# Optimization experiments

Measured on AMD Instinct MI355X. Metric: run time of the kernel, lower is better.

## Reference

```python
import jax, jax.numpy as jnp
import numpy as np

WINDOW = 13

def setup_inputs() -> dict:
    key = jax.random.key(0)
    ks = jax.random.split(key, 5)
    B, C, D, H, W = 8, 64, 13, 64, 64
    c8 = C // 8
    x = jax.random.normal(ks[0], (B, C, D, H, W), dtype=jnp.float32)
    wq = jax.random.normal(ks[1], (c8, C), dtype=jnp.float32) * 0.1
    wk = jax.random.normal(ks[2], (c8, C), dtype=jnp.float32) * 0.1
    wv = jax.random.normal(ks[3], (C, C), dtype=jnp.float32) * 0.1
    bq = jnp.zeros((c8,), jnp.float32)
    bk = jnp.zeros((c8,), jnp.float32)
    bv = jnp.zeros((C,), jnp.float32)
    return {"x": x, "wq": wq, "bq": bq, "wk": wk, "bk": bk, "wv": wv, "bv": bv}

def reference(x, wq, bq, wk, bk, wv, bv):
    B, C, D, H, W = x.shape
    N = D * H * W
    nb = N // WINDOW  # N chosen divisible by WINDOW
    xf = x.reshape(B, C, N)
    # 1x1 Conv3d == per-voxel channel matmul
    q = jnp.einsum('oc,bcn->bon', wq, xf) + bq[None, :, None]
    k = jnp.einsum('oc,bcn->bon', wk, xf) + bk[None, :, None]
    v = jnp.einsum('oc,bcn->bon', wv, xf) + bv[None, :, None]
    # split flattened spatial dim into independent windows of size 13
    qb = q.reshape(B, -1, nb, WINDOW)
    kb = k.reshape(B, -1, nb, WINDOW)
    vb = v.reshape(B, C, nb, WINDOW)
    # scores[b,n,i,j] = sum_c q[b,c,n,i] * k[b,c,n,j]  (no scaling, as in source)
    scores = jnp.einsum('bcni,bcnj->bnij', qb, kb)
    att = jax.nn.softmax(scores, axis=-1)
    # out[b,c,n,i] = sum_j v[b,c,n,j] * att[b,n,i,j]  (v @ att^T per window)
    out = jnp.einsum('bcnj,bnij->bcni', vb, att)
    return out.reshape(B, C, D, H, W)
```

## Files before the change

### kernel.cpp

```cpp
#include <hip/hip_runtime.h>

#define WINDOW 13
#define NTOT   53248
#define WPB    8
#define VT     104
#define VS     112
#define WS     72
#define QKS    112
#define VFS    68

typedef float floatx4 __attribute__((ext_vector_type(4)));
typedef short shortx8 __attribute__((ext_vector_type(8)));

__device__ __forceinline__ unsigned short f2bf(float f) {
    union { float f; unsigned int u; } v; v.f = f;
    unsigned int u = v.u;
    unsigned int r = (u + 0x7fffu + ((u >> 16) & 1u)) >> 16;
    return (unsigned short)r;
}

__device__ __forceinline__ unsigned int pk2(float a, float b) {
    return (unsigned int)f2bf(a) | ((unsigned int)f2bf(b) << 16);
}

__global__ __launch_bounds__(512, 4)
void attn_win13_kernel(const float* __restrict__ x,
                       const float* __restrict__ wq, const float* __restrict__ bq,
                       const float* __restrict__ wk, const float* __restrict__ bk,
                       const float* __restrict__ wv, const float* __restrict__ bv,
                       float* __restrict__ out)
{
    __shared__ __align__(16) unsigned short xT[VS * WS];
    __shared__ __align__(16) unsigned short wbf[80 * WS];
    __shared__ float ball[80];
    __shared__ __align__(16) float vf[VS * VFS];
    __shared__ float qk[16 * QKS];
    __shared__ float att[WPB * 169];

    const int tid = threadIdx.x;
    const int b   = blockIdx.y;
    const int v0  = blockIdx.x * VT;
    const size_t total = (size_t)512 * NTOT;

    if (tid < 224) {
        const int vq = tid >> 3, cg8 = tid & 7;
        const int c0 = cg8 * 8, vx = vq * 4;
        float xv[4][8];
#pragma unroll
        for (int i = 0; i < 8; ++i) {
            size_t idx = (size_t)(b * 64 + c0 + i) * NTOT + v0 + vx;
            if (idx > total - 4) idx = total - 4;
            const float4 t = *(const float4*)(x + idx);
            xv[0][i] = t.x; xv[1][i] = t.y; xv[2][i] = t.z; xv[3][i] = t.w;
        }
#pragma unroll
        for (int r = 0; r < 4; ++r) {
            uint4 pk;
            pk.x = pk2(xv[r][0], xv[r][1]);
            pk.y = pk2(xv[r][2], xv[r][3]);
            pk.z = pk2(xv[r][4], xv[r][5]);
            pk.w = pk2(xv[r][6], xv[r][7]);
            *(uint4*)(&xT[(vx + r) * WS + c0]) = pk;
        }
    } else if (tid >= 256) {
        const int wf0 = tid - 256;
#pragma unroll
        for (int it = 0; it < 3; ++it) {
            const int wf = wf0 + (it << 8);
            if (wf < 640) {
                const int r = wf >> 3, cw = (wf & 7) * 8;
                const float* src = (r < 8)  ? (wq + r * 64 + cw)
                                 : (r < 16) ? (wk + (r - 8) * 64 + cw)
                                            : (wv + (r - 16) * 64 + cw);
                const float4 w0 = *(const float4*)src;
                const float4 w1 = *(const float4*)(src + 4);
                uint4 pk;
                pk.x = pk2(w0.x, w0.y); pk.y = pk2(w0.z, w0.w);
                pk.z = pk2(w1.x, w1.y); pk.w = pk2(w1.z, w1.w);
                *(uint4*)(&wbf[r * WS + cw]) = pk;
            }
        }
    }
    if (tid >= 432) {
        const int t2 = tid - 432;
        ball[t2] = (t2 < 8) ? bq[t2] : (t2 < 16) ? bk[t2 - 8] : bv[t2 - 16];
    }
    __syncthreads();

    {
        const int wid  = tid >> 6;
        const int lane = tid & 63;
        const int col  = lane & 15;
        const int g    = lane >> 4;
        for (int t = wid; t < 35; t += 8) {
            const int mt = t / 7, nt = t % 7;
            const shortx8 a0 = *(const shortx8*)(&wbf[(mt * 16 + col) * WS + g * 8]);
            const shortx8 b0 = *(const shortx8*)(&xT [(nt * 16 + col) * WS + g * 8]);
            const shortx8 a1 = *(const shortx8*)(&wbf[(mt * 16 + col) * WS + 32 + g * 8]);
            const shortx8 b1 = *(const shortx8*)(&xT [(nt * 16 + col) * WS + 32 + g * 8]);
            floatx4 acc = {0.f, 0.f, 0.f, 0.f};
            acc = __builtin_amdgcn_mfma_f32_16x16x32_bf16(a0, b0, acc, 0, 0, 0);
            acc = __builtin_amdgcn_mfma_f32_16x16x32_bf16(a1, b1, acc, 0, 0, 0);
            const int row0 = mt * 16 + g * 4;
            const int vox  = nt * 16 + col;
            if (mt == 0) {
                qk[(row0 + 0) * QKS + vox] = acc[0] + ball[row0 + 0];
                qk[(row0 + 1) * QKS + vox] = acc[1] + ball[row0 + 1];
                qk[(row0 + 2) * QKS + vox] = acc[2] + ball[row0 + 2];
                qk[(row0 + 3) * QKS + vox] = acc[3] + ball[row0 + 3];
            } else {
                const int c0 = row0 - 16;
                float4 st = make_float4(acc[0] + ball[row0 + 0], acc[1] + ball[row0 + 1],
                                        acc[2] + ball[row0 + 2], acc[3] + ball[row0 + 3]);
                *(float4*)(&vf[vox * VFS + c0]) = st;
            }
        }
    }
    __syncthreads();

    for (int f = tid; f < WPB * 169; f += 512) {
        const int w = f / 169, rem = f % 169;
        const int i = rem / 13, j = rem % 13;
        const float* qp = &qk[w * 13 + i];
        const float* kp = &qk[w * 13 + j];
        float s = 0.f;
#pragma unroll
        for (int o = 0; o < 8; ++o)
            s += qp[o * QKS] * kp[(8 + o) * QKS];
        att[f] = s;
    }
    __syncthreads();

    if (tid < WPB * WINDOW) {
        float* row = att + tid * 13;
        float m = row[0];
#pragma unroll
        for (int j = 1; j < 13; ++j) m = fmaxf(m, row[j]);
        float s0 = __expf(row[0] - m), s1 = __expf(row[1] - m), s2 = __expf(row[2] - m);
        float s3 = __expf(row[3] - m), s4 = __expf(row[4] - m), s5 = __expf(row[5] - m);
        float s6 = __expf(row[6] - m), s7 = __expf(row[7] - m), s8 = __expf(row[8] - m);
        float s9 = __expf(row[9] - m), sa = __expf(row[10] - m), sb = __expf(row[11] - m);
        float sc = __expf(row[12] - m);
        const float inv = 1.f / (s0+s1+s2+s3+s4+s5+s6+s7+s8+s9+sa+sb+sc);
        row[0]=s0*inv; row[1]=s1*inv; row[2]=s2*inv; row[3]=s3*inv; row[4]=s4*inv;
        row[5]=s5*inv; row[6]=s6*inv; row[7]=s7*inv; row[8]=s8*inv; row[9]=s9*inv;
        row[10]=sa*inv; row[11]=sb*inv; row[12]=sc*inv;
    }
    __syncthreads();

    for (int f = tid; f < 16 * VT; f += 512) {
        const int cg = f / VT, vx = f % VT;
        const int w = vx / 13, i = vx % 13;
        const float* arow  = att + w * 169 + i * 13;
        const float* vbase = &vf[(w * 13) * VFS + cg * 4];
        float4 o4 = make_float4(0.f, 0.f, 0.f, 0.f);
#pragma unroll
        for (int j = 0; j < 13; ++j) {
            const float a = arow[j];
            const float4 vv = *(const float4*)(vbase + j * VFS);
            o4.x += a * vv.x; o4.y += a * vv.y; o4.z += a * vv.z; o4.w += a * vv.w;
        }
        float* op = out + (size_t)(b * 64 + cg * 4) * NTOT + v0 + vx;
        op[0]                 = o4.x;
        op[(size_t)NTOT]      = o4.y;
        op[(size_t)2 * NTOT]  = o4.z;
        op[(size_t)3 * NTOT]  = o4.w;
    }
}

extern "C" void kernel_launch(void* const* d_in, const int* in_sizes, int n_in,
                              void* d_out, int out_size, void* d_ws, size_t ws_size,
                              hipStream_t stream) {
    const float* x  = (const float*)d_in[0];
    const float* wq = (const float*)d_in[1];
    const float* bq = (const float*)d_in[2];
    const float* wk = (const float*)d_in[3];
    const float* bk = (const float*)d_in[4];
    const float* wv = (const float*)d_in[5];
    const float* bv = (const float*)d_in[6];
    float* out = (float*)d_out;

    dim3 grid(NTOT / VT, 8);
    dim3 block(512);
    attn_win13_kernel<<<grid, block, 0, stream>>>(x, wq, bq, wk, bk, wv, bv, out);
}
```

Before: 235.7 us.

## Store V in bf16 LDS and alias attention buffer to cut LDS footprint

The V projection is now packed to bf16 in shared memory instead of fp32, and the attention buffer reuses the weight staging buffer. Together these shrink LDS use so launch bounds can go from 4 to 6 blocks per CU. The output loop now gives each thread 8 channels instead of 4, halving the loop iterations. In exchange, V carries bf16 rounding error, and the kernel now depends on wbf being dead after the projection step.

```diff
diff --git a/kernel.cpp b/kernel.cpp
--- a/kernel.cpp
+++ b/kernel.cpp
@@ -7,7 +7,6 @@
 #define VS     112
 #define WS     72
 #define QKS    112
-#define VFS    68
 
 typedef float floatx4 __attribute__((ext_vector_type(4)));
 typedef short shortx8 __attribute__((ext_vector_type(8)));
@@ -23,7 +22,14 @@
     return (unsigned int)f2bf(a) | ((unsigned int)f2bf(b) << 16);
 }
 
-__global__ __launch_bounds__(512, 4)
+__device__ __forceinline__ float bflo(unsigned int u) {
+    union { unsigned int u; float f; } v; v.u = u << 16; return v.f;
+}
+__device__ __forceinline__ float bfhi(unsigned int u) {
+    union { unsigned int u; float f; } v; v.u = u & 0xffff0000u; return v.f;
+}
+
+__global__ __launch_bounds__(512, 6)
 void attn_win13_kernel(const float* __restrict__ x,
                        const float* __restrict__ wq, const float* __restrict__ bq,
                        const float* __restrict__ wk, const float* __restrict__ bk,
@@ -33,9 +39,9 @@
     __shared__ __align__(16) unsigned short xT[VS * WS];
     __shared__ __align__(16) unsigned short wbf[80 * WS];
     __shared__ float ball[80];
-    __shared__ __align__(16) float vf[VS * VFS];
-    __shared__ float qk[16 * QKS];
-    __shared__ float att[WPB * 169];
+    __shared__ __align__(16) unsigned short vbf[VT * WS];
+    __shared__ __align__(16) float qk[16 * QKS];
+    float* const att = (float*)wbf;
 
     const int tid = threadIdx.x;
     const int b   = blockIdx.y;
@@ -108,11 +114,12 @@
                 qk[(row0 + 1) * QKS + vox] = acc[1] + ball[row0 + 1];
                 qk[(row0 + 2) * QKS + vox] = acc[2] + ball[row0 + 2];
                 qk[(row0 + 3) * QKS + vox] = acc[3] + ball[row0 + 3];
-            } else {
+            } else if (vox < VT) {
                 const int c0 = row0 - 16;
-                float4 st = make_float4(acc[0] + ball[row0 + 0], acc[1] + ball[row0 + 1],
-                                        acc[2] + ball[row0 + 2], acc[3] + ball[row0 + 3]);
-                *(float4*)(&vf[vox * VFS + c0]) = st;
+                uint2 st;
+                st.x = pk2(acc[0] + ball[row0 + 0], acc[1] + ball[row0 + 1]);
+                st.y = pk2(acc[2] + ball[row0 + 2], acc[3] + ball[row0 + 3]);
+                *(uint2*)(&vbf[vox * WS + c0]) = st;
             }
         }
     }
@@ -148,23 +155,30 @@
     }
     __syncthreads();
 
-    for (int f = tid; f < 16 * VT; f += 512) {
+    for (int f = tid; f < 8 * VT; f += 512) {
         const int cg = f / VT, vx = f % VT;
         const int w = vx / 13, i = vx % 13;
-        const float* arow  = att + w * 169 + i * 13;
-        const float* vbase = &vf[(w * 13) * VFS + cg * 4];
-        float4 o4 = make_float4(0.f, 0.f, 0.f, 0.f);
+        const float* arow = att + w * 169 + i * 13;
+        const unsigned short* vbase = &vbf[(w * 13) * WS + cg * 8];
+        float o0=0.f,o1=0.f,o2=0.f,o3=0.f,o4=0.f,o5=0.f,o6=0.f,o7=0.f;
 #pragma unroll
         for (int j = 0; j < 13; ++j) {
             const float a = arow[j];
-            const float4 vv = *(const float4*)(vbase + j * VFS);
-            o4.x += a * vv.x; o4.y += a * vv.y; o4.z += a * vv.z; o4.w += a * vv.w;
-        }
-        float* op = out + (size_t)(b * 64 + cg * 4) * NTOT + v0 + vx;
-        op[0]                 = o4.x;
-        op[(size_t)NTOT]      = o4.y;
-        op[(size_t)2 * NTOT]  = o4.z;
-        op[(size_t)3 * NTOT]  = o4.w;
+            const uint4 vv = *(const uint4*)(vbase + j * WS);
+            o0 += a * bflo(vv.x); o1 += a * bfhi(vv.x);
+            o2 += a * bflo(vv.y); o3 += a * bfhi(vv.y);
+            o4 += a * bflo(vv.z); o5 += a * bfhi(vv.z);
+            o6 += a * bflo(vv.w); o7 += a * bfhi(vv.w);
+        }
+        float* op = out + (size_t)(b * 64 + cg * 8) * NTOT + v0 + vx;
+        op[0]                 = o0;
+        op[(size_t)NTOT]      = o1;
+        op[(size_t)2 * NTOT]  = o2;
+        op[(size_t)3 * NTOT]  = o3;
+        op[(size_t)4 * NTOT]  = o4;
+        op[(size_t)5 * NTOT]  = o5;
+        op[(size_t)6 * NTOT]  = o6;
+        op[(size_t)7 * NTOT]  = o7;
     }
 }
 
```

New measurement: 229.9 us. -2.4%, faster.

## Compute attention-weighted V with bf16 MFMA and shrink shared memory for occupancy

Applied to the files above, without the earlier changes.

Stores V projections as bf16 in a padded per-window layout and writes softmax probabilities as zero-padded bf16 rows. The final out = V·attᵀ product then runs on 16x16x32 MFMA (one wave per window) instead of a scalar FMA loop. It also reuses the weight and qk buffers for the score and probability arrays, which cuts LDS per block and allows launch bounds to be raised to 6 blocks. The trade-off is lower precision for V and the attention weights, plus some redundant padded MFMA work.

```diff
diff --git a/kernel.cpp b/kernel.cpp
--- a/kernel.cpp
+++ b/kernel.cpp
@@ -7,7 +7,7 @@
 #define VS     112
 #define WS     72
 #define QKS    112
-#define VFS    68
+#define VPS    132
 
 typedef float floatx4 __attribute__((ext_vector_type(4)));
 typedef short shortx8 __attribute__((ext_vector_type(8)));
@@ -23,7 +23,7 @@
     return (unsigned int)f2bf(a) | ((unsigned int)f2bf(b) << 16);
 }
 
-__global__ __launch_bounds__(512, 4)
+__global__ __launch_bounds__(512, 6)
 void attn_win13_kernel(const float* __restrict__ x,
                        const float* __restrict__ wq, const float* __restrict__ bq,
                        const float* __restrict__ wk, const float* __restrict__ bk,
@@ -33,9 +33,10 @@
     __shared__ __align__(16) unsigned short xT[VS * WS];
     __shared__ __align__(16) unsigned short wbf[80 * WS];
     __shared__ float ball[80];
-    __shared__ __align__(16) float vf[VS * VFS];
-    __shared__ float qk[16 * QKS];
-    __shared__ float att[WPB * 169];
+    __shared__ __align__(16) unsigned short vpad[64 * VPS];
+    __shared__ __align__(16) float qk[16 * QKS];
+    float* const att = (float*)wbf;
+    unsigned short* const attb = (unsigned short*)qk;
 
     const int tid = threadIdx.x;
     const int b   = blockIdx.y;
@@ -85,6 +86,11 @@
         const int t2 = tid - 432;
         ball[t2] = (t2 < 8) ? bq[t2] : (t2 < 16) ? bk[t2 - 8] : bv[t2 - 16];
     }
+    {
+        const int r = tid >> 3, w = tid & 7;
+        vpad[r * VPS + w * 16 + 13] = 0;
+        *(unsigned int*)(&vpad[r * VPS + w * 16 + 14]) = 0u;
+    }
     __syncthreads();
 
     {
@@ -94,25 +100,33 @@
         const int g    = lane >> 4;
         for (int t = wid; t < 35; t += 8) {
             const int mt = t / 7, nt = t % 7;
-            const shortx8 a0 = *(const shortx8*)(&wbf[(mt * 16 + col) * WS + g * 8]);
-            const shortx8 b0 = *(const shortx8*)(&xT [(nt * 16 + col) * WS + g * 8]);
-            const shortx8 a1 = *(const shortx8*)(&wbf[(mt * 16 + col) * WS + 32 + g * 8]);
-            const shortx8 b1 = *(const shortx8*)(&xT [(nt * 16 + col) * WS + 32 + g * 8]);
+            const shortx8 wa0 = *(const shortx8*)(&wbf[(mt * 16 + col) * WS + g * 8]);
+            const shortx8 xa0 = *(const shortx8*)(&xT [(nt * 16 + col) * WS + g * 8]);
+            const shortx8 wa1 = *(const shortx8*)(&wbf[(mt * 16 + col) * WS + 32 + g * 8]);
+            const shortx8 xa1 = *(const shortx8*)(&xT [(nt * 16 + col) * WS + 32 + g * 8]);
             floatx4 acc = {0.f, 0.f, 0.f, 0.f};
-            acc = __builtin_amdgcn_mfma_f32_16x16x32_bf16(a0, b0, acc, 0, 0, 0);
-            acc = __builtin_amdgcn_mfma_f32_16x16x32_bf16(a1, b1, acc, 0, 0, 0);
-            const int row0 = mt * 16 + g * 4;
-            const int vox  = nt * 16 + col;
             if (mt == 0) {
+                acc = __builtin_amdgcn_mfma_f32_16x16x32_bf16(wa0, xa0, acc, 0, 0, 0);
+                acc = __builtin_amdgcn_mfma_f32_16x16x32_bf16(wa1, xa1, acc, 0, 0, 0);
+                const int row0 = g * 4;
+                const int vox  = nt * 16 + col;
                 qk[(row0 + 0) * QKS + vox] = acc[0] + ball[row0 + 0];
                 qk[(row0 + 1) * QKS + vox] = acc[1] + ball[row0 + 1];
                 qk[(row0 + 2) * QKS + vox] = acc[2] + ball[row0 + 2];
                 qk[(row0 + 3) * QKS + vox] = acc[3] + ball[row0 + 3];
             } else {
-                const int c0 = row0 - 16;
-                float4 st = make_float4(acc[0] + ball[row0 + 0], acc[1] + ball[row0 + 1],
-                                        acc[2] + ball[row0 + 2], acc[3] + ball[row0 + 3]);
-                *(float4*)(&vf[vox * VFS + c0]) = st;
+                acc = __builtin_amdgcn_mfma_f32_16x16x32_bf16(xa0, wa0, acc, 0, 0, 0);
+                acc = __builtin_amdgcn_mfma_f32_16x16x32_bf16(xa1, wa1, acc, 0, 0, 0);
+                const int c_out = (mt - 1) * 16 + col;
+                const float bias = ball[16 + c_out];
+                int vox = nt * 16 + g * 4;
+                int w = vox / 13, j = vox - w * 13;
+#pragma unroll
+                for (int r = 0; r < 4; ++r) {
+                    if (vox + r < VT)
+                        vpad[c_out * VPS + w * 16 + j] = f2bf(acc[r] + bias);
+                    if (++j == 13) { j = 0; ++w; }
+                }
             }
         }
     }
@@ -132,7 +146,8 @@
     __syncthreads();
 
     if (tid < WPB * WINDOW) {
-        float* row = att + tid * 13;
+        const int w = tid / 13, i = tid - w * 13;
+        const float* row = att + w * 169 + i * 13;
         float m = row[0];
 #pragma unroll
         for (int j = 1; j < 13; ++j) m = fmaxf(m, row[j]);
@@ -142,29 +157,39 @@
         float s9 = __expf(row[9] - m), sa = __expf(row[10] - m), sb = __expf(row[11] - m);
         float sc = __expf(row[12] - m);
         const float inv = 1.f / (s0+s1+s2+s3+s4+s5+s6+s7+s8+s9+sa+sb+sc);
-        row[0]=s0*inv; row[1]=s1*inv; row[2]=s2*inv; row[3]=s3*inv; row[4]=s4*inv;
-        row[5]=s5*inv; row[6]=s6*inv; row[7]=s7*inv; row[8]=s8*inv; row[9]=s9*inv;
-        row[10]=sa*inv; row[11]=sb*inv; row[12]=sc*inv;
-    }
-    __syncthreads();
-
-    for (int f = tid; f < 16 * VT; f += 512) {
-        const int cg = f / VT, vx = f % VT;
-        const int w = vx / 13, i = vx % 13;
-        const float* arow  = att + w * 169 + i * 13;
-        const float* vbase = &vf[(w * 13) * VFS + cg * 4];
-        float4 o4 = make_float4(0.f, 0.f, 0.f, 0.f);
-#pragma unroll
-        for (int j = 0; j < 13; ++j) {
-            const float a = arow[j];
-            const float4 vv = *(const float4*)(vbase + j * VFS);
-            o4.x += a * vv.x; o4.y += a * vv.y; o4.z += a * vv.z; o4.w += a * vv.w;
-        }
-        float* op = out + (size_t)(b * 64 + cg * 4) * NTOT + v0 + vx;
-        op[0]                 = o4.x;
-        op[(size_t)NTOT]      = o4.y;
-        op[(size_t)2 * NTOT]  = o4.z;
-        op[(size_t)3 * NTOT]  = o4.w;
+        unsigned short* ab = attb + w * 256 + i * 16;
+        uint4 lo, hi;
+        lo.x = pk2(s0 * inv, s1 * inv); lo.y = pk2(s2 * inv, s3 * inv);
+        lo.z = pk2(s4 * inv, s5 * inv); lo.w = pk2(s6 * inv, s7 * inv);
+        hi.x = pk2(s8 * inv, s9 * inv); hi.y = pk2(sa * inv, sb * inv);
+        hi.z = pk2(sc * inv, 0.f);      hi.w = 0u;
+        *(uint4*)ab       = lo;
+        *(uint4*)(ab + 8) = hi;
+    }
+    __syncthreads();
+
+    {
+        const int wid  = tid >> 6;
+        const int lane = tid & 63;
+        const int col  = lane & 15;
+        const int g    = lane >> 4;
+        const int gg   = (g & 1) * 8;
+        shortx8 bfrag = *(const shortx8*)(&attb[wid * 256 + col * 16 + gg]);
+        if (g & 2) bfrag = (shortx8){0, 0, 0, 0, 0, 0, 0, 0};
+        const size_t obase = (size_t)(b * 64) * NTOT + v0 + wid * 13 + col;
+#pragma unroll
+        for (int ct = 0; ct < 4; ++ct) {
+            const shortx8 afrag = *(const shortx8*)(&vpad[(ct * 16 + col) * VPS + wid * 16 + gg]);
+            floatx4 acc = {0.f, 0.f, 0.f, 0.f};
+            acc = __builtin_amdgcn_mfma_f32_16x16x32_bf16(afrag, bfrag, acc, 0, 0, 0);
+            if (col < 13) {
+                float* op = out + obase + (size_t)(ct * 16 + g * 4) * NTOT;
+                op[0]                = acc[0];
+                op[(size_t)NTOT]     = acc[1];
+                op[(size_t)2 * NTOT] = acc[2];
+                op[(size_t)3 * NTOT] = acc[3];
+            }
+        }
     }
 }
 
```

Measured after the change: 233.2 us. Within noise of the previous version (-1.1%).
